# Kernel tuning notes

Hardware: AMD Instinct MI355X
Metric: run time of the kernel (lower is better)

## Reference

```python
import jax, jax.numpy as jnp
import numpy as np

C, P, E = 2048, 128, 2048          # clusters, max points per cluster, edges
N = C * P                          # total voxels
COORD_LO, COORD_HI = 1, 4          # coords_col


def setup_inputs() -> dict:
    key = jax.random.key(0)
    k1, k2, k3 = jax.random.split(key, 3)
    data = jax.random.normal(k1, (N, 8), dtype=jnp.float32)
    # disjoint clusters: contiguous index blocks of size P
    clusts = jnp.arange(N, dtype=jnp.int32).reshape(C, P)
    # valid point count per cluster in [64, 128]
    clust_sizes = jax.random.randint(k2, (C,), 64, P + 1, dtype=jnp.int32)
    edge_index = jax.random.randint(k3, (2, E), 0, C, dtype=jnp.int32)
    return {"data": data, "clusts": clusts, "clust_sizes": clust_sizes,
            "edge_index": edge_index}


def reference(data, clusts, clust_sizes, edge_index):
    # directed branch of ClustGeoEdgeEncoder (random edges -> undirected=False)
    coords = data[:, COORD_LO:COORD_HI]                 # [N, 3]
    pts = coords[clusts]                                # [C, P, 3]
    valid = jnp.arange(P)[None, :] < clust_sizes[:, None]  # [C, P]

    src, dst = edge_index[0], edge_index[1]
    x1, x2 = pts[src], pts[dst]                         # [E, P, 3]
    m1, m2 = valid[src], valid[dst]                     # [E, P]

    # pairwise squared Euclidean distances via gram trick (avoids [E,P,P,3])
    sq1 = jnp.sum(x1 * x1, axis=-1)                     # [E, P]
    sq2 = jnp.sum(x2 * x2, axis=-1)
    inner = jnp.einsum('epd,eqd->epq', x1, x2)          # [E, P, P]
    d2 = sq1[:, :, None] + sq2[:, None, :] - 2.0 * inner
    d2 = jnp.maximum(d2, 0.0)
    pair_ok = m1[:, :, None] & m2[:, None, :]
    d2 = jnp.where(pair_ok, d2, jnp.inf)

    # argmin over the flattened local distance matrix, as in the torch loop
    imin = jnp.argmin(d2.reshape(E, P * P), axis=1)
    i1, i2 = imin // P, imin % P
    er = jnp.arange(E)
    v1 = x1[er, i1]                                     # [E, 3] closest point in c1
    v2 = x2[er, i2]                                     # [E, 3] closest point in c2

    disp = v1 - v2
    lend = jnp.linalg.norm(disp, axis=-1)               # [E]
    safe = jnp.where(lend > 0, lend, 1.0)[:, None]
    disp = jnp.where(lend[:, None] > 0, disp / safe, disp)
    B = (disp[:, :, None] * disp[:, None, :]).reshape(E, 9)  # outer product

    return jnp.concatenate([v1, v2, disp, lend[:, None], B], axis=1)  # [E, 19]
```

## Files before the change

### kernel.cpp

```cpp
#include <hip/hip_runtime.h>
#include <math.h>

#define CC 2048
#define PP 128
#define EE 2048

__global__ __launch_bounds__(256) void clust_geo_edge_kernel(
    const float* __restrict__ data,
    const int*   __restrict__ clusts,
    const int*   __restrict__ clust_sizes,
    const int*   __restrict__ edge_index,
    float*       __restrict__ out)
{
    __shared__ float4 s1[PP];
    __shared__ float4 s2[PP];
    __shared__ float  red_v[4];
    __shared__ int    red_i[4];

    const int e = blockIdx.x;
    const int t = threadIdx.x;

    const int src = edge_index[e];
    const int dst = edge_index[EE + e];
    const int n1  = clust_sizes[src];
    const int n2  = clust_sizes[dst];

    {
        const int which = t >> 7;
        const int p = t & (PP - 1);
        const int c = which ? dst : src;
        const int n = which ? n2 : n1;
        const int pt = c * PP + p;
        float4 v = *reinterpret_cast<const float4*>(data + (size_t)pt * 8);
        const float x = v.y, y = v.z, z = v.w;
        const float sq = __fadd_rn(__fadd_rn(__fmul_rn(x, x), __fmul_rn(y, y)),
                                   __fmul_rn(z, z));
        const float w = (p < n) ? sq : INFINITY;
        float4 o;
        if (which) {
            o.x = -2.0f * x; o.y = -2.0f * y; o.z = -2.0f * z; o.w = w;
            s2[p] = o;
        } else {
            o.x = x; o.y = y; o.z = z; o.w = w;
            s1[p] = o;
        }
    }
    __syncthreads();

    const int qid  = t & 31;
    const int pgid = t >> 5;

    const bool q2 = (n2 > 64);
    const bool q3 = (n2 > 96);

    const float4 b0 = s2[qid];
    const float4 b1 = s2[qid + 32];
    float4 b2, b3;
    if (q2) b2 = s2[qid + 64];
    if (q3) b3 = s2[qid + 96];

    float bv0 = INFINITY, bv1 = INFINITY;
    int   br0 = 0,        br1 = 0;

    auto evalp = [](const float4& A, const float4& B, float& bv, int& br,
                    const int r) {
        const float m2i = __fadd_rn(
            __fadd_rn(__fmul_rn(B.x, A.x), __fmul_rn(B.y, A.y)),
            __fmul_rn(B.z, A.z));
        const float d2 = __fadd_rn(__fadd_rn(A.w, B.w), m2i);
        const float nv = __builtin_amdgcn_fmed3f(d2, 0.0f, bv);
        if (nv < bv) br = r;
        bv = nv;
    };

    auto evalrow = [&](const int mi) {
        const float4 A = s1[pgid + 8 * mi];
        evalp(A, b0, bv0, br0, mi * 2 + 0);
        evalp(A, b1, bv1, br1, mi * 2 + 0);
        if (q2) evalp(A, b2, bv0, br0, mi * 2 + 1);
        if (q3) evalp(A, b3, bv1, br1, mi * 2 + 1);
    };

    evalrow(0);  evalrow(1);  evalrow(2);  evalrow(3);
    evalrow(4);  evalrow(5);  evalrow(6);  evalrow(7);
    if (n1 >  64) evalrow(8);
    if (n1 >  72) evalrow(9);
    if (n1 >  80) evalrow(10);
    if (n1 >  88) evalrow(11);
    if (n1 >  96) evalrow(12);
    if (n1 > 104) evalrow(13);
    if (n1 > 112) evalrow(14);
    if (n1 > 120) evalrow(15);

    const int f0 = (pgid + 8 * (br0 >> 1)) * PP + (qid + 32 * ((br0 & 1) * 2));
    const int f1 = (pgid + 8 * (br1 >> 1)) * PP + (qid + 32 * ((br1 & 1) * 2 + 1));

    float best_v = bv0;
    int   best_i = f0;
    if (bv1 < best_v || (bv1 == best_v && f1 < best_i)) {
        best_v = bv1; best_i = f1;
    }

    #pragma unroll
    for (int off = 32; off > 0; off >>= 1) {
        const float ov = __shfl_down(best_v, off);
        const int   oi = __shfl_down(best_i, off);
        if (ov < best_v || (ov == best_v && oi < best_i)) {
            best_v = ov; best_i = oi;
        }
    }
    const int wave = t >> 6;
    if ((t & 63) == 0) { red_v[wave] = best_v; red_i[wave] = best_i; }
    __syncthreads();

    if (t == 0) {
        float fv = red_v[0]; int fi = red_i[0];
        #pragma unroll
        for (int w = 1; w < 4; ++w) {
            const float ov = red_v[w]; const int oi = red_i[w];
            if (ov < fv || (ov == fv && oi < fi)) { fv = ov; fi = oi; }
        }
        const int i1 = fi >> 7;
        const int i2 = fi & (PP - 1);
        const float4 A  = s1[i1];
        const float4 Bq = s2[i2];
        const float bx = __fmul_rn(Bq.x, -0.5f);
        const float by = __fmul_rn(Bq.y, -0.5f);
        const float bz = __fmul_rn(Bq.z, -0.5f);

        const float d0 = __fsub_rn(A.x, bx);
        const float d1 = __fsub_rn(A.y, by);
        const float d2 = __fsub_rn(A.z, bz);
        const float ss = __fadd_rn(__fadd_rn(__fmul_rn(d0, d0), __fmul_rn(d1, d1)),
                                   __fmul_rn(d2, d2));
        const float lend = __fsqrt_rn(ss);

        float u0 = d0, u1 = d1, u2 = d2;
        if (lend > 0.0f) {
            u0 = __fdiv_rn(d0, lend);
            u1 = __fdiv_rn(d1, lend);
            u2 = __fdiv_rn(d2, lend);
        }

        float* o = out + (size_t)e * 19;
        o[0] = A.x; o[1] = A.y; o[2] = A.z;
        o[3] = bx;  o[4] = by;  o[5] = bz;
        o[6] = u0;  o[7] = u1;  o[8] = u2;
        o[9] = lend;
        o[10] = __fmul_rn(u0, u0); o[11] = __fmul_rn(u0, u1); o[12] = __fmul_rn(u0, u2);
        o[13] = __fmul_rn(u1, u0); o[14] = __fmul_rn(u1, u1); o[15] = __fmul_rn(u1, u2);
        o[16] = __fmul_rn(u2, u0); o[17] = __fmul_rn(u2, u1); o[18] = __fmul_rn(u2, u2);
    }
}

extern "C" void kernel_launch(void* const* d_in, const int* in_sizes, int n_in,
                              void* d_out, int out_size, void* d_ws, size_t ws_size,
                              hipStream_t stream) {
    const float* data        = (const float*)d_in[0];
    const int*   clusts      = (const int*)d_in[1];
    const int*   clust_sizes = (const int*)d_in[2];
    const int*   edge_index  = (const int*)d_in[3];
    float*       out         = (float*)d_out;

    clust_geo_edge_kernel<<<EE, 256, 0, stream>>>(data, clusts, clust_sizes,
                                                  edge_index, out);
}
```

Measured before the change: 15.15 us.

## Use packed FP32 math with SoA shared layout for pairwise distances

```diff
diff --git a/kernel.cpp b/kernel.cpp
--- a/kernel.cpp
+++ b/kernel.cpp
@@ -4,6 +4,15 @@
 #define CC 2048
 #define PP 128
 #define EE 2048
+
+typedef float f32x2 __attribute__((ext_vector_type(2)));
+
+__device__ __forceinline__ f32x2 pk_mul(f32x2 a, f32x2 b) {
+    f32x2 d; asm("v_pk_mul_f32 %0, %1, %2" : "=v"(d) : "v"(a), "v"(b)); return d;
+}
+__device__ __forceinline__ f32x2 pk_add(f32x2 a, f32x2 b) {
+    f32x2 d; asm("v_pk_add_f32 %0, %1, %2" : "=v"(d) : "v"(a), "v"(b)); return d;
+}
 
 __global__ __launch_bounds__(256) void clust_geo_edge_kernel(
     const float* __restrict__ data,
@@ -13,7 +22,10 @@
     float*       __restrict__ out)
 {
     __shared__ float4 s1[PP];
-    __shared__ float4 s2[PP];
+    __shared__ __align__(16) float s2x[PP];
+    __shared__ __align__(16) float s2y[PP];
+    __shared__ __align__(16) float s2z[PP];
+    __shared__ __align__(16) float s2w[PP];
     __shared__ float  red_v[4];
     __shared__ int    red_i[4];
 
@@ -36,12 +48,11 @@
         const float sq = __fadd_rn(__fadd_rn(__fmul_rn(x, x), __fmul_rn(y, y)),
                                    __fmul_rn(z, z));
         const float w = (p < n) ? sq : INFINITY;
-        float4 o;
         if (which) {
-            o.x = -2.0f * x; o.y = -2.0f * y; o.z = -2.0f * z; o.w = w;
-            s2[p] = o;
+            s2x[p] = -2.0f * x; s2y[p] = -2.0f * y;
+            s2z[p] = -2.0f * z; s2w[p] = w;
         } else {
-            o.x = x; o.y = y; o.z = z; o.w = w;
+            float4 o; o.x = x; o.y = y; o.z = z; o.w = w;
             s1[p] = o;
         }
     }
@@ -49,36 +60,51 @@
 
     const int qid  = t & 31;
     const int pgid = t >> 5;
+    const int q0   = 2 * qid;
 
     const bool q2 = (n2 > 64);
-    const bool q3 = (n2 > 96);
 
-    const float4 b0 = s2[qid];
-    const float4 b1 = s2[qid + 32];
-    float4 b2, b3;
-    if (q2) b2 = s2[qid + 64];
-    if (q3) b3 = s2[qid + 96];
+    const f32x2 B0x = *reinterpret_cast<const f32x2*>(&s2x[q0]);
+    const f32x2 B0y = *reinterpret_cast<const f32x2*>(&s2y[q0]);
+    const f32x2 B0z = *reinterpret_cast<const f32x2*>(&s2z[q0]);
+    const f32x2 B0w = *reinterpret_cast<const f32x2*>(&s2w[q0]);
+    f32x2 B1x, B1y, B1z, B1w;
+    if (q2) {
+        B1x = *reinterpret_cast<const f32x2*>(&s2x[q0 + 64]);
+        B1y = *reinterpret_cast<const f32x2*>(&s2y[q0 + 64]);
+        B1z = *reinterpret_cast<const f32x2*>(&s2z[q0 + 64]);
+        B1w = *reinterpret_cast<const f32x2*>(&s2w[q0 + 64]);
+    }
 
     float bv0 = INFINITY, bv1 = INFINITY;
     int   br0 = 0,        br1 = 0;
 
-    auto evalp = [](const float4& A, const float4& B, float& bv, int& br,
-                    const int r) {
-        const float m2i = __fadd_rn(
-            __fadd_rn(__fmul_rn(B.x, A.x), __fmul_rn(B.y, A.y)),
-            __fmul_rn(B.z, A.z));
-        const float d2 = __fadd_rn(__fadd_rn(A.w, B.w), m2i);
-        const float nv = __builtin_amdgcn_fmed3f(d2, 0.0f, bv);
-        if (nv < bv) br = r;
-        bv = nv;
+    auto evalfrag = [&](const f32x2& Bx, const f32x2& By, const f32x2& Bz,
+                        const f32x2& Bw, const f32x2& Ax, const f32x2& Ay,
+                        const f32x2& Az, const f32x2& Aw, const int r) {
+        const f32x2 t1  = pk_mul(Bx, Ax);
+        const f32x2 t2  = pk_mul(By, Ay);
+        const f32x2 s   = pk_add(t1, t2);
+        const f32x2 t3  = pk_mul(Bz, Az);
+        const f32x2 m2i = pk_add(s, t3);
+        const f32x2 sq  = pk_add(Bw, Aw);
+        const f32x2 d2  = pk_add(sq, m2i);
+        const float nv0 = __builtin_amdgcn_fmed3f(d2.x, 0.0f, bv0);
+        if (nv0 < bv0) br0 = r;
+        bv0 = nv0;
+        const float nv1 = __builtin_amdgcn_fmed3f(d2.y, 0.0f, bv1);
+        if (nv1 < bv1) br1 = r;
+        bv1 = nv1;
     };
 
     auto evalrow = [&](const int mi) {
         const float4 A = s1[pgid + 8 * mi];
-        evalp(A, b0, bv0, br0, mi * 2 + 0);
-        evalp(A, b1, bv1, br1, mi * 2 + 0);
-        if (q2) evalp(A, b2, bv0, br0, mi * 2 + 1);
-        if (q3) evalp(A, b3, bv1, br1, mi * 2 + 1);
+        const f32x2 Ax = {A.x, A.x};
+        const f32x2 Ay = {A.y, A.y};
+        const f32x2 Az = {A.z, A.z};
+        const f32x2 Aw = {A.w, A.w};
+        evalfrag(B0x, B0y, B0z, B0w, Ax, Ay, Az, Aw, mi * 2 + 0);
+        if (q2) evalfrag(B1x, B1y, B1z, B1w, Ax, Ay, Az, Aw, mi * 2 + 1);
     };
 
     evalrow(0);  evalrow(1);  evalrow(2);  evalrow(3);
@@ -92,8 +118,8 @@
     if (n1 > 112) evalrow(14);
     if (n1 > 120) evalrow(15);
 
-    const int f0 = (pgid + 8 * (br0 >> 1)) * PP + (qid + 32 * ((br0 & 1) * 2));
-    const int f1 = (pgid + 8 * (br1 >> 1)) * PP + (qid + 32 * ((br1 & 1) * 2 + 1));
+    const int f0 = (pgid + 8 * (br0 >> 1)) * PP + (q0 + 64 * (br0 & 1));
+    const int f1 = (pgid + 8 * (br1 >> 1)) * PP + (q0 + 1 + 64 * (br1 & 1));
 
     float best_v = bv0;
     int   best_i = f0;
@@ -122,11 +148,10 @@
         }
         const int i1 = fi >> 7;
         const int i2 = fi & (PP - 1);
-        const float4 A  = s1[i1];
-        const float4 Bq = s2[i2];
-        const float bx = __fmul_rn(Bq.x, -0.5f);
-        const float by = __fmul_rn(Bq.y, -0.5f);
-        const float bz = __fmul_rn(Bq.z, -0.5f);
+        const float4 A = s1[i1];
+        const float bx = __fmul_rn(s2x[i2], -0.5f);
+        const float by = __fmul_rn(s2y[i2], -0.5f);
+        const float bz = __fmul_rn(s2z[i2], -0.5f);
 
         const float d0 = __fsub_rn(A.x, bx);
         const float d1 = __fsub_rn(A.y, by);
```

New measurement: 15.47 us. +2.1%, slower.
